# Kernel optimization log

Hardware: AMD Instinct MI355X
Metric: run time of the kernel (lower is better)

## Reference

```python
import jax, jax.numpy as jnp
import numpy as np

N = 20000      # total nodes
E = 160000     # total edges
G = 64         # graphs in batch
D_ESM = 1280
D = 512
OUT = 500
NUM_LAYERS = 3


def setup_inputs() -> dict:
    key = jax.random.key(0)
    ks = jax.random.split(key, 16)
    s = 0.02
    inp = {
        "native_x": jax.random.randint(ks[0], (N,), 0, 21),
        "x": jax.random.normal(ks[1], (N, D_ESM), dtype=jnp.float32),
        "edge_index": jax.random.randint(ks[2], (2, E), 0, N),
        "batch": jnp.sort(jax.random.randint(ks[3], (N,), 0, G)),
        # parameters
        "embed_table": jax.random.normal(ks[4], (21, 96), dtype=jnp.float32) * s,
        "proj_aa_w": jax.random.normal(ks[5], (96, D), dtype=jnp.float32) * s,
        "proj_aa_b": jnp.zeros((D,), jnp.float32),
        "proj_esm_w": jax.random.normal(ks[6], (D_ESM, D), dtype=jnp.float32) * s,
        "proj_esm_b": jnp.zeros((D,), jnp.float32),
        "gcn_w": jax.random.normal(ks[7], (NUM_LAYERS, D, D), dtype=jnp.float32) * s,
        "gcn_b": jnp.zeros((NUM_LAYERS, D), jnp.float32),
        "ro1_w": jax.random.normal(ks[8], (D, 1024), dtype=jnp.float32) * s,
        "ro1_b": jnp.zeros((1024,), jnp.float32),
        "ro2_w": jax.random.normal(ks[9], (1024, OUT), dtype=jnp.float32) * s,
        "ro2_b": jnp.zeros((OUT,), jnp.float32),
        "weight1": jnp.array([0.6, 0.4], jnp.float32),
    }
    return inp


def _gcn_stack(feat, src, dst, enorm, self_norm, gcn_w, gcn_b):
    # GraphCNN: 3 GCNConv layers (PyG: sym-normalized adj with self loops),
    # residual add after the first layer.
    for i in range(NUM_LAYERS):
        hW = feat @ gcn_w[i]                                   # [N, D]
        msg = hW[src] * enorm[:, None]                          # [E, D] gather
        agg = jax.ops.segment_sum(msg, dst, num_segments=N)     # scatter-add
        agg = agg + hW * self_norm[:, None] + gcn_b[i]
        out = jax.nn.relu(agg)
        feat = out if i == 0 else feat + out
    return feat


def reference(native_x, x, edge_index, batch, embed_table,
              proj_aa_w, proj_aa_b, proj_esm_w, proj_esm_b,
              gcn_w, gcn_b, ro1_w, ro1_b, ro2_w, ro2_b, weight1):
    # embedding + projections (dropout = identity, eval mode)
    x_aa = embed_table[native_x] @ proj_aa_w + proj_aa_b        # [N, 512]
    x_esm_lin = x @ proj_esm_w + proj_esm_b                     # [N, 512]
    h = jax.nn.relu(x_aa + x_esm_lin)
    x_esm = jax.nn.relu(x_esm_lin)

    src, dst = edge_index[0], edge_index[1]
    # GCN normalization with self loops: deg over targets + 1
    deg = jax.ops.segment_sum(jnp.ones((E,), x.dtype), dst, num_segments=N) + 1.0
    dis = deg ** -0.5
    enorm = dis[src] * dis[dst]     # per-edge norm
    self_norm = dis * dis           # self-loop norm

    n1 = _gcn_stack(h, src, dst, enorm, self_norm, gcn_w, gcn_b)
    n3 = _gcn_stack(x_esm, src, dst, enorm, self_norm, gcn_w, gcn_b)

    # global max pool per graph
    g1 = jax.ops.segment_max(n1, batch, num_segments=G)          # [G, 512]
    g3 = jax.ops.segment_max(n3, batch, num_segments=G)

    g = weight1[0] * g1 + weight1[1] * g3
    y = jax.nn.sigmoid(jax.nn.relu(g @ ro1_w + ro1_b) @ ro2_w + ro2_b)
    return y
```

## Files before the change

kernel.cpp:

```cpp
#include <hip/hip_runtime.h>
#include <float.h>

#define NN 20000
#define EE 160000
#define GG 64
#define DD 512
#define NL 3
#define M2 40000
#define M2P 40960
#define M1 20000
#define M1P 20480
#define BK 64

typedef __bf16 bf16x8 __attribute__((ext_vector_type(8)));
typedef float f32x4 __attribute__((ext_vector_type(4)));
typedef unsigned int u32;
typedef unsigned short u16;
typedef u32 u32x4 __attribute__((ext_vector_type(4)));
typedef u32 u32x2 __attribute__((ext_vector_type(2)));

union FragU { u32x4 u; bf16x8 b; };

__device__ inline float blo(u32 u){ union{u32 i;float f;}x; x.i=u<<16; return x.f; }
__device__ inline float bhi(u32 u){ union{u32 i;float f;}x; x.i=u&0xFFFF0000u; return x.f; }
__device__ inline u16 f2bf(float f){ union{float f;u32 i;}x; x.f=f; u32 r=x.i+0x7FFFu+((x.i>>16)&1u); return (u16)(r>>16); }
__device__ inline u32 pack2(float a,float b){ return (u32)f2bf(a) | ((u32)f2bf(b)<<16); }

__device__ __forceinline__ void gload16(const void* g, void* lds){
  __builtin_amdgcn_global_load_lds(
    (const __attribute__((address_space(1))) void*)g,
    (__attribute__((address_space(3))) void*)lds, 16, 0, 0);
}

__device__ __forceinline__ void acc8(float* a, uint4 q, float w){
  a[0]+=w*blo(q.x); a[1]+=w*bhi(q.x);
  a[2]+=w*blo(q.y); a[3]+=w*bhi(q.y);
  a[4]+=w*blo(q.z); a[5]+=w*bhi(q.z);
  a[6]+=w*blo(q.w); a[7]+=w*bhi(q.w);
}

__global__ void k_cvtdeg(const float* __restrict__ in, u16* __restrict__ outp,
                         const int* __restrict__ ei, int* __restrict__ deg){
  int b = blockIdx.x;
  if(b < 12800){
    int t = b*256+threadIdx.x;
    int row = t/160, gidx = t%160;
    u32x4 o;
    if(row < M1){
      const float* s = in + (size_t)row*1280 + gidx*8;
      float4 v0 = *(const float4*)s;
      float4 v1 = *(const float4*)(s+4);
      o.x=pack2(v0.x,v0.y); o.y=pack2(v0.z,v0.w);
      o.z=pack2(v1.x,v1.y); o.w=pack2(v1.z,v1.w);
    } else {
      o.x=o.y=o.z=o.w=0u;
    }
    *(u32x4*)(outp + (size_t)row*1280 + gidx*8) = o;
  } else {
    int e = (b-12800)*256+threadIdx.x;
    if(e<EE) atomicAdd(&deg[ei[EE+e]], 1);
  }
}

__device__ __forceinline__ void dev_tcvt(const float* __restrict__ in, u16* __restrict__ outp,
                                         int R, int C, int bx, int by, int tx, int ty, float* t){
  int c0 = bx*32, r0 = by*32;
  t[ty*33+tx] = in[(size_t)(r0+ty)*C + c0+tx];
  __syncthreads();
  outp[(size_t)(c0+ty)*R + r0+tx] = f2bf(t[tx*33+ty]);
}
__device__ __forceinline__ void dev_t32(const float* __restrict__ in, float* __restrict__ outp,
                                        int R, int C, int bx, int by, int tx, int ty, float* t){
  int c0 = bx*32, r0 = by*32;
  int r = r0+ty, c = c0+tx;
  if(r<R && c<C) t[ty*33+tx] = in[(size_t)r*C + c];
  __syncthreads();
  int oc = c0+ty, orr = r0+tx;
  if(oc<C && orr<R) outp[(size_t)oc*R + orr] = t[tx*33+ty];
}

__global__ __launch_bounds__(1024) void k_prep(const float* __restrict__ pesm_w, u16* __restrict__ WtE,
    const float* __restrict__ gcn_w, u16* __restrict__ WtG,
    const float* __restrict__ ro1_w, float* __restrict__ roT1,
    const float* __restrict__ ro2_w, float* __restrict__ roT2,
    const float* __restrict__ et, const float* __restrict__ paa_w,
    const float* __restrict__ paa_b, float* __restrict__ embp){
  __shared__ float t[32*33];
  int rb = blockIdx.x;
  int tid = threadIdx.x;
  int tx = tid&31, ty = tid>>5;
  if(rb < 640){ dev_tcvt(pesm_w, WtE, 1280, 512, rb%16, rb/16, tx, ty, t); return; }
  rb -= 640;
  if(rb < 768){
    int z = rb/256, r2 = rb%256;
    dev_tcvt(gcn_w + (size_t)z*262144, WtG + (size_t)z*262144, 512, 512, r2%16, r2/16, tx, ty, t);
    return;
  }
  rb -= 768;
  if(rb < 512){ dev_t32(ro1_w, roT1, 512, 1024, rb%32, rb/32, tx, ty, t); return; }
  rb -= 512;
  if(rb < 512){ dev_t32(ro2_w, roT2, 1024, 500, rb%16, rb/16, tx, ty, t); return; }
  rb -= 512;
  {
    int tt = rb*1024 + tid;
    if(tt < 21*512){
      int a = tt>>9, d = tt&511;
      float s = paa_b[d];
      for(int k=0;k<96;k++) s += et[a*96+k]*paa_w[k*512+d];
      embp[tt] = s;
    }
  }
}

__global__ __launch_bounds__(1024) void k_scanA(const int* __restrict__ deg, int* __restrict__ loff,
                        float* __restrict__ dis, const int* __restrict__ batch,
                        int* __restrict__ starts, int* __restrict__ bsum){
  __shared__ int ws[16];
  int b = blockIdx.x, tid = threadIdx.x;
  int n = b*1024 + tid;
  int lane = tid & 63, wv = tid >> 6;
  int dv = 0;
  if(n < NN){ dv = deg[n]; dis[n] = rsqrtf((float)dv + 1.0f); }
  int v = dv;
  #pragma unroll
  for(int off=1; off<64; off<<=1){
    int t = __shfl_up(v, off, 64);
    if(lane >= off) v += t;
  }
  if(lane==63) ws[wv] = v;
  __syncthreads();
  if(wv==0){
    int s = (lane<16)? ws[lane] : 0;
    #pragma unroll
    for(int off=1; off<16; off<<=1){
      int t = __shfl_up(s, off, 64);
      if(lane>=off) s += t;
    }
    if(lane<16) ws[lane] = s;
  }
  __syncthreads();
  int wbase = wv ? ws[wv-1] : 0;
  if(n < NN) loff[n] = wbase + v - dv;
  if(tid==1023) bsum[b] = ws[15];
  if(n < NN){
    int bb = batch[n];
    int pb = n ? batch[n-1] : -1;
    for(int g=pb+1; g<=bb; g++) starts[g]=n;
    if(n==NN-1){ for(int g=bb+1; g<=GG; g++) starts[g]=NN; }
  }
}
__global__ void k_scanB(const int* __restrict__ bsum, int* __restrict__ bbase){
  int lane = threadIdx.x;
  int x = (lane<20)? bsum[lane] : 0;
  int v = x;
  #pragma unroll
  for(int off=1; off<32; off<<=1){
    int t = __shfl_up(v, off, 64);
    if(lane>=off) v += t;
  }
  if(lane<20) bbase[lane] = v - x;
}
__global__ void k_scanC(const int* __restrict__ loff, const int* __restrict__ bbase,
                        int* __restrict__ offs){
  int n = blockIdx.x*1024 + threadIdx.x;
  if(n < NN) offs[n] = bbase[n>>10] + loff[n];
  if(n == 0) offs[NN] = EE;
}
__global__ void k_fill(const int* __restrict__ ei, const int* __restrict__ offs, int* __restrict__ curs,
                       const float* __restrict__ dis, int2* __restrict__ edat){
  int e = blockIdx.x*256+threadIdx.x; if(e>=EE) return;
  int s = ei[e], d = ei[EE+e];
  int pos = atomicAdd(&curs[d],1);
  edat[offs[d]+pos] = make_int2(s*2048, __float_as_int(dis[s]*dis[d]));
}

template<int EPI>
__global__ __launch_bounds__(256) void k_gemm(const u16* __restrict__ A, const u16* __restrict__ Bt,
                                              u16* __restrict__ C, int Mstore, int K, int lda,
                                              const int* __restrict__ nx, const float* __restrict__ embp,
                                              const float* __restrict__ esm_b){
  __shared__ u16 lsA[128*BK];
  __shared__ u16 lsB[128*BK];
  const int tid = threadIdx.x;
  const int lane = tid & 63;
  const int wid = tid >> 6;
  const int wr = wid >> 1, wc = wid & 1;
  const int la = lane & 15, lg = lane >> 4;
  const int w = blockIdx.x;
  const int xr = w & 7, kk2 = w >> 3;
  const int n0 = (kk2 & 3) * 128;
  const int rowB = (xr + 8*(kk2 >> 2)) * 128;

  f32x4 acc[4][4];
  #pragma unroll
  for(int m=0;m<4;m++)
    #pragma unroll
    for(int n=0;n<4;n++)
      #pragma unroll
      for(int r=0;r<4;r++) acc[m][n][r]=0.f;

  const u16* Arow = A + (size_t)rowB*lda;
  const u16* Brow = Bt + (size_t)n0*K;

  int srow[4], scol[4], ldsoff[4];
  #pragma unroll
  for(int i=0;i<4;i++){
    int li = i*256+tid;
    srow[i] = li>>3;
    scol[i] = ((li&7) ^ (srow[i]&7))*8;
    ldsoff[i] = (i*256 + wid*64)*8;
  }

  for(int k0=0;k0<K;k0+=BK){
    #pragma unroll
    for(int i=0;i<4;i++)
      gload16(Arow + (size_t)srow[i]*lda + k0 + scol[i], lsA + ldsoff[i]);
    #pragma unroll
    for(int i=0;i<4;i++)
      gload16(Brow + (size_t)srow[i]*K + k0 + scol[i], lsB + ldsoff[i]);
    __syncthreads();
    #pragma unroll
    for(int kk=0;kk<2;kk++){
      FragU aF[4], bF[4];
      #pragma unroll
      for(int m=0;m<4;m++){
        int row = wr*64+m*16+la;
        aF[m].u = *(const u32x4*)&lsA[row*BK + ((kk*4+lg)^(row&7))*8];
      }
      #pragma unroll
      for(int n=0;n<4;n++){
        int row = wc*64+n*16+la;
        bF[n].u = *(const u32x4*)&lsB[row*BK + ((kk*4+lg)^(row&7))*8];
      }
      #pragma unroll
      for(int m=0;m<4;m++)
        #pragma unroll
        for(int n=0;n<4;n++)
          acc[m][n] = __builtin_amdgcn_mfma_f32_16x16x32_bf16(aF[m].b, bF[n].b, acc[m][n], 0,0,0);
    }
    __syncthreads();
  }
  #pragma unroll
  for(int m=0;m<4;m++)
    #pragma unroll
    for(int r=0;r<4;r++){
      int rr = rowB + wr*64 + m*16 + lg*4 + r;
      if(rr < Mstore){
        int aidx = (EPI==1) ? nx[rr] : 0;
        #pragma unroll
        for(int n=0;n<4;n++){
          int col = n0 + wc*64 + n*16 + la;
          float v = acc[m][n][r];
          if(EPI==0){
            C[(size_t)rr*512 + col] = f2bf(v);
          } else {
            float t1 = v + esm_b[col];
            float hh = embp[aidx*512 + col] + t1;
            C[(size_t)(2*rr)*512 + col]   = f2bf(hh>0.f?hh:0.f);
            C[(size_t)(2*rr+1)*512 + col] = f2bf(t1>0.f?t1:0.f);
          }
        }
      }
    }
}

template<int MODE>
__global__ __launch_bounds__(256) void k_agg7(const u16* __restrict__ hW, u16* __restrict__ feat,
                 const int* __restrict__ offs, const int2* __restrict__ edat,
                 const float* __restrict__ dis, const float* __restrict__ bias){
  const int b = blockIdx.x;
  const int sl = b & 1;
  const int wv = threadIdx.x >> 6;
  const int lane = threadIdx.x & 63;
  const int nn = (b>>1)*4 + wv;
  const int co = sl*1024 + lane*16;
  const char* base = (const char*)hW;
  const int e0 = offs[nn], e1 = offs[nn+1];
  float a[8]={0,0,0,0,0,0,0,0};

  uint4 qs = *(const uint4*)(base + (size_t)nn*2048 + co);
  uint4 qf = make_uint4(0,0,0,0);
  if(MODE>0) qf = *(const uint4*)((const char*)feat + (size_t)nn*2048 + co);
  float dn = dis[nn], sn = dn*dn;

  int e = e0;
  for(; e+1 < e1; e += 2){
    int2 edA = edat[e], edB = edat[e+1];
    uint4 qA = *(const uint4*)(base + (u32)edA.x + co);
    uint4 qB = *(const uint4*)(base + (u32)edB.x + co);
    acc8(a, qA, __int_as_float(edA.y));
    acc8(a, qB, __int_as_float(edB.y));
  }
  if(e < e1){
    int2 edA = edat[e];
    uint4 qA = *(const uint4*)(base + (u32)edA.x + co);
    acc8(a, qA, __int_as_float(edA.y));
  }
  acc8(a, qs, sn);

  float4 b0 = *(const float4*)(bias + lane*8);
  float4 b1 = *(const float4*)(bias + lane*8 + 4);
  a[0]+=b0.x; a[1]+=b0.y; a[2]+=b0.z; a[3]+=b0.w;
  a[4]+=b1.x; a[5]+=b1.y; a[6]+=b1.z; a[7]+=b1.w;
  #pragma unroll
  for(int j=0;j<8;j++) a[j] = a[j]>0.f ? a[j] : 0.f;
  if(MODE>0) acc8(a, qf, 1.f);
  uint4 o;
  o.x=pack2(a[0],a[1]); o.y=pack2(a[2],a[3]);
  o.z=pack2(a[4],a[5]); o.w=pack2(a[6],a[7]);
  *(uint4*)((char*)feat + (size_t)nn*2048 + co) = o;
}

__global__ void k_pool(const u16* __restrict__ feat, const int* __restrict__ starts,
                       u32* __restrict__ m1, u32* __restrict__ m3){
  int g = blockIdx.x, c = blockIdx.y;
  int s = starts[g], e = starts[g+1];
  int len = e - s;
  int b0 = s + (len*c)/8, b1 = s + (len*(c+1))/8;
  int t = threadIdx.x;
  float a0=0.f, a1=0.f, c0=0.f, c1=0.f;
  for(int n=b0;n<b1;++n){
    const u16* pr = feat + (size_t)(2*n)*512 + t*2;
    u32 q1 = *(const u32*)pr;
    u32 q3 = *(const u32*)(pr + 512);
    a0 = fmaxf(a0, blo(q1)); a1 = fmaxf(a1, bhi(q1));
    c0 = fmaxf(c0, blo(q3)); c1 = fmaxf(c1, bhi(q3));
  }
  atomicMax(m1 + g*512 + t*2,     __float_as_uint(a0));
  atomicMax(m1 + g*512 + t*2 + 1, __float_as_uint(a1));
  atomicMax(m3 + g*512 + t*2,     __float_as_uint(c0));
  atomicMax(m3 + g*512 + t*2 + 1, __float_as_uint(c1));
}

__global__ __launch_bounds__(256) void k_ro1v(const u32* __restrict__ m1b, const u32* __restrict__ m3b,
                                              const float* __restrict__ w1, const float* __restrict__ wT,
                                              const float* __restrict__ b, float* __restrict__ r1){
  int gw = blockIdx.x*4 + (threadIdx.x>>6);
  int g = gw >> 10, o = gw & 1023;
  int lane = threadIdx.x & 63;
  float w10 = w1[0], w11 = w1[1];
  const uint4* g1 = (const uint4*)(m1b + (size_t)g*512);
  const uint4* g3 = (const uint4*)(m3b + (size_t)g*512);
  const float4* wr = (const float4*)(wT + (size_t)o*512);
  float s = 0.f;
  #pragma unroll
  for(int i=0;i<2;i++){
    uint4 q1 = g1[i*64+lane];
    uint4 q3 = g3[i*64+lane];
    float4 w = wr[i*64+lane];
    s += (w10*__uint_as_float(q1.x) + w11*__uint_as_float(q3.x))*w.x;
    s += (w10*__uint_as_float(q1.y) + w11*__uint_as_float(q3.y))*w.y;
    s += (w10*__uint_as_float(q1.z) + w11*__uint_as_float(q3.z))*w.z;
    s += (w10*__uint_as_float(q1.w) + w11*__uint_as_float(q3.w))*w.w;
  }
  #pragma unroll
  for(int m=32;m>=1;m>>=1) s += __shfl_xor(s, m, 64);
  if(lane==0){ s += b[o]; r1[gw] = s>0.f ? s : 0.f; }
}
__global__ __launch_bounds__(256) void k_ro2v(const float* __restrict__ r1, const float* __restrict__ wT,
                                              const float* __restrict__ b, float* __restrict__ y){
  int gw = blockIdx.x*4 + (threadIdx.x>>6);
  int g = gw/500, o = gw - g*500;
  int lane = threadIdx.x & 63;
  const float4* gr = (const float4*)(r1 + (size_t)g*1024);
  const float4* wr = (const float4*)(wT + (size_t)o*1024);
  float s = 0.f;
  #pragma unroll
  for(int i=0;i<4;i++){
    float4 a = gr[i*64+lane];
    float4 w = wr[i*64+lane];
    s += a.x*w.x + a.y*w.y + a.z*w.z + a.w*w.w;
  }
  #pragma unroll
  for(int m=32;m>=1;m>>=1) s += __shfl_xor(s, m, 64);
  if(lane==0) y[gw] = 1.0f/(1.0f+__expf(-(s + b[o])));
}

extern "C" void kernel_launch(void* const* d_in, const int* in_sizes, int n_in,
                              void* d_out, int out_size, void* d_ws, size_t ws_size,
                              hipStream_t stream){
  const int*   native_x = (const int*)d_in[0];
  const float* x        = (const float*)d_in[1];
  const int*   ei       = (const int*)d_in[2];
  const int*   batch    = (const int*)d_in[3];
  const float* embed_t  = (const float*)d_in[4];
  const float* paa_w    = (const float*)d_in[5];
  const float* paa_b    = (const float*)d_in[6];
  const float* pesm_w   = (const float*)d_in[7];
  const float* pesm_b   = (const float*)d_in[8];
  const float* gcn_w    = (const float*)d_in[9];
  const float* gcn_b    = (const float*)d_in[10];
  const float* ro1_w    = (const float*)d_in[11];
  const float* ro1_b    = (const float*)d_in[12];
  const float* ro2_w    = (const float*)d_in[13];
  const float* ro2_b    = (const float*)d_in[14];
  const float* w1       = (const float*)d_in[15];
  float* out = (float*)d_out;

  char* p = (char*)d_ws;
  auto alloc = [&](size_t n){ void* r = (void*)p; p += (n + 255) & ~(size_t)255; return r; };
  u16* feat   = (u16*)alloc((size_t)M2P*512*2);
  u16* hW     = (u16*)alloc((size_t)M2P*512*2);
  u16* xbf    = (u16*)alloc((size_t)M1P*1280*2);
  u16* WtE    = (u16*)alloc((size_t)512*1280*2);
  u16* WtG    = (u16*)alloc((size_t)3*512*512*2);
  float* roT1 = (float*)alloc((size_t)1024*512*4);
  float* roT2 = (float*)alloc((size_t)500*1024*4);
  float* embp = (float*)alloc(21*512*4);
  int* deg    = (int*)alloc(NN*4);
  int* curs   = (int*)alloc(NN*4);
  float* dis  = (float*)alloc(NN*4);
  int* loff   = (int*)alloc(NN*4);
  int* offs   = (int*)alloc((NN+1)*4);
  int* bsum   = (int*)alloc(32*4);
  int* bbase  = (int*)alloc(32*4);
  int2* edat  = (int2*)alloc((size_t)EE*8);
  int* starts = (int*)alloc((GG+1)*4);
  u32* m1b    = (u32*)alloc(GG*512*4);
  u32* m3b    = (u32*)alloc(GG*512*4);
  float* r1   = (float*)alloc(GG*1024*4);
  (void)ws_size; (void)in_sizes; (void)n_in; (void)out_size;

  hipMemsetAsync(deg, 0, ((NN*4+255)&~(size_t)255) + NN*4, stream);
  hipMemsetAsync(m1b, 0, 2*GG*512*4, stream);

  k_cvtdeg<<<12800+625,256,0,stream>>>(x, xbf, ei, deg);
  k_prep<<<640+768+512+512+11,1024,0,stream>>>(pesm_w, WtE, gcn_w, WtG, ro1_w, roT1, ro2_w, roT2,
                                               embed_t, paa_w, paa_b, embp);
  k_scanA<<<20,1024,0,stream>>>(deg, loff, dis, batch, starts, bsum);
  k_scanB<<<1,64,0,stream>>>(bsum, bbase);
  k_scanC<<<20,1024,0,stream>>>(loff, bbase, offs);
  k_fill<<<(EE+255)/256,256,0,stream>>>(ei, offs, curs, dis, edat);

  k_gemm<1><<<4*(M1P/128),256,0,stream>>>(xbf, WtE, feat, M1, 1280, 1280, native_x, embp, pesm_b);

  k_gemm<0><<<4*(M2P/128),256,0,stream>>>(feat, WtG,            hW, M2, 512, 512, nullptr, nullptr, nullptr);
  k_agg7<0><<<NN/2,256,0,stream>>>(hW, feat, offs, edat, dis, gcn_b);
  k_gemm<0><<<4*(M2P/128),256,0,stream>>>(feat, WtG+262144,     hW, M2, 512, 512, nullptr, nullptr, nullptr);
  k_agg7<1><<<NN/2,256,0,stream>>>(hW, feat, offs, edat, dis, gcn_b+512);
  k_gemm<0><<<4*(M2P/128),256,0,stream>>>(feat, WtG+2*262144,   hW, M2, 512, 512, nullptr, nullptr, nullptr);
  k_agg7<1><<<NN/2,256,0,stream>>>(hW, feat, offs, edat, dis, gcn_b+1024);

  k_pool<<<dim3(GG,8),256,0,stream>>>(feat, starts, m1b, m3b);
  k_ro1v<<<16384,256,0,stream>>>(m1b, m3b, w1, roT1, ro1_b, r1);
  k_ro2v<<<8000,256,0,stream>>>(r1, roT2, ro2_b, out);
}
```

Baseline: 398.2 us.

## Rewrite GEMM as 256x256-tile, 8-wave kernel with double-buffered LDS pipeline

Result: slower. 437.4 us (+9.8%).

```diff
diff --git a/kernel.cpp b/kernel.cpp
--- a/kernel.cpp
+++ b/kernel.cpp
@@ -174,77 +174,127 @@
   edat[offs[d]+pos] = make_int2(s*2048, __float_as_int(dis[s]*dis[d]));
 }
 
+#define ASM_VMCNT4 asm volatile("s_waitcnt vmcnt(4)" ::: "memory")
+#define ASM_VMCNT0 asm volatile("s_waitcnt vmcnt(0)" ::: "memory")
+#define ASM_LGKM0  asm volatile("s_waitcnt lgkmcnt(0)" ::: "memory")
+
 template<int EPI>
-__global__ __launch_bounds__(256) void k_gemm(const u16* __restrict__ A, const u16* __restrict__ Bt,
+__global__ __launch_bounds__(512,2) void k_gemm8(const u16* __restrict__ A, const u16* __restrict__ Bt,
                                               u16* __restrict__ C, int Mstore, int K, int lda,
                                               const int* __restrict__ nx, const float* __restrict__ embp,
                                               const float* __restrict__ esm_b){
-  __shared__ u16 lsA[128*BK];
-  __shared__ u16 lsB[128*BK];
+  __shared__ u16 ls[8*8192];
   const int tid = threadIdx.x;
   const int lane = tid & 63;
   const int wid = tid >> 6;
-  const int wr = wid >> 1, wc = wid & 1;
+  const int wr = wid >> 2;
+  const int wc = wid & 3;
   const int la = lane & 15, lg = lane >> 4;
   const int w = blockIdx.x;
   const int xr = w & 7, kk2 = w >> 3;
-  const int n0 = (kk2 & 3) * 128;
-  const int rowB = (xr + 8*(kk2 >> 2)) * 128;
-
-  f32x4 acc[4][4];
-  #pragma unroll
-  for(int m=0;m<4;m++)
+  const int n0 = (kk2 & 1) * 256;
+  const int rowB = (xr + 8*(kk2 >> 1)) * 256;
+  const int nt = K >> 6;
+
+  const u16* Arow = A + (size_t)rowB*lda;
+  const u16* Brow = Bt + (size_t)n0*K;
+
+  f32x4 acc[8][4];
+  #pragma unroll
+  for(int m=0;m<8;m++)
     #pragma unroll
     for(int n=0;n<4;n++)
       #pragma unroll
       for(int r=0;r<4;r++) acc[m][n][r]=0.f;
 
-  const u16* Arow = A + (size_t)rowB*lda;
-  const u16* Brow = Bt + (size_t)n0*K;
-
-  int srow[4], scol[4], ldsoff[4];
-  #pragma unroll
-  for(int i=0;i<4;i++){
-    int li = i*256+tid;
-    srow[i] = li>>3;
-    scol[i] = ((li&7) ^ (srow[i]&7))*8;
-    ldsoff[i] = (i*256 + wid*64)*8;
-  }
-
-  for(int k0=0;k0<K;k0+=BK){
-    #pragma unroll
-    for(int i=0;i<4;i++)
-      gload16(Arow + (size_t)srow[i]*lda + k0 + scol[i], lsA + ldsoff[i]);
-    #pragma unroll
-    for(int i=0;i<4;i++)
-      gload16(Brow + (size_t)srow[i]*K + k0 + scol[i], lsB + ldsoff[i]);
-    __syncthreads();
-    #pragma unroll
-    for(int kk=0;kk<2;kk++){
-      FragU aF[4], bF[4];
-      #pragma unroll
-      for(int m=0;m<4;m++){
-        int row = wr*64+m*16+la;
-        aF[m].u = *(const u32x4*)&lsA[row*BK + ((kk*4+lg)^(row&7))*8];
-      }
-      #pragma unroll
-      for(int n=0;n<4;n++){
-        int row = wc*64+n*16+la;
-        bF[n].u = *(const u32x4*)&lsB[row*BK + ((kk*4+lg)^(row&7))*8];
-      }
-      #pragma unroll
-      for(int m=0;m<4;m++)
-        #pragma unroll
-        for(int n=0;n<4;n++)
-          acc[m][n] = __builtin_amdgcn_mfma_f32_16x16x32_bf16(aF[m].b, bF[n].b, acc[m][n], 0,0,0);
-    }
-    __syncthreads();
-  }
-  #pragma unroll
-  for(int m=0;m<4;m++)
+  int srow[2], sgc[2];
+  #pragma unroll
+  for(int j=0;j<2;j++){
+    int s = j*512+tid;
+    srow[j] = s>>2;
+    sgc[j]  = ((s&3) ^ ((srow[j]>>1)&3))*8;
+  }
+
+#define PANEL(buf,mat,kh) (ls + (((buf)*2+(mat))*2+(kh))*8192)
+#define STAGE(buf,mat,kh,kt) { \
+    const u16* _src = (mat)? Brow : Arow; \
+    int _ld = (mat)? K : lda; \
+    int _k0 = (kt)*64 + (kh)*32; \
+    u16* _dst = PANEL(buf,mat,kh); \
+    _Pragma("unroll") \
+    for(int _j=0;_j<2;_j++) \
+      gload16(_src + (size_t)srow[_j]*_ld + _k0 + sgc[_j], _dst + (_j*512+tid)*8); \
+  }
+#define LDA4(f,buf,kh,qm) { \
+    const u16* _pa = PANEL(buf,0,kh); \
+    _Pragma("unroll") \
+    for(int _m=0;_m<4;_m++){ \
+      int _row = wr*128 + (qm)*64 + _m*16 + la; \
+      f[_m].u = *(const u32x4*)(_pa + _row*32 + ((lg ^ ((_row>>1)&3))*8)); \
+    } \
+  }
+#define LDB4(f,buf,kh) { \
+    const u16* _pb = PANEL(buf,1,kh); \
+    _Pragma("unroll") \
+    for(int _n=0;_n<4;_n++){ \
+      int _row = wc*64 + _n*16 + la; \
+      f[_n].u = *(const u32x4*)(_pb + _row*32 + ((lg ^ ((_row>>1)&3))*8)); \
+    } \
+  }
+#define MM16(af,bf,qm) { \
+    _Pragma("unroll") \
+    for(int _m=0;_m<4;_m++) \
+      _Pragma("unroll") \
+      for(int _n=0;_n<4;_n++) \
+        acc[(qm)*4+_m][_n] = __builtin_amdgcn_mfma_f32_16x16x32_bf16(af[_m].b, bf[_n].b, acc[(qm)*4+_m][_n], 0,0,0); \
+  }
+
+  STAGE(0,0,0,0); STAGE(0,1,0,0); STAGE(0,0,1,0); STAGE(0,1,1,0);
+  ASM_VMCNT4;
+  __builtin_amdgcn_s_barrier();
+
+  for(int t=0;t<nt;t++){
+    const int c = t&1;
+    const bool st = (t+1 < nt);
+    const bool lastt = (t == nt-1);
+    FragU aF[4], b0F[4], b1F[4];
+
+    LDA4(aF, c, 0, 0); LDB4(b0F, c, 0);
+    if(st) STAGE(c^1, 0, 0, t+1);
+    __builtin_amdgcn_s_barrier();
+    ASM_LGKM0; __builtin_amdgcn_sched_barrier(0);
+    __builtin_amdgcn_s_setprio(1); MM16(aF, b0F, 0); __builtin_amdgcn_s_setprio(0);
+    __builtin_amdgcn_s_barrier();
+
+    LDA4(aF, c, 0, 1);
+    if(st) STAGE(c^1, 1, 0, t+1);
+    if(lastt){ ASM_VMCNT0; } else { ASM_VMCNT4; }
+    __builtin_amdgcn_s_barrier();
+    ASM_LGKM0; __builtin_amdgcn_sched_barrier(0);
+    __builtin_amdgcn_s_setprio(1); MM16(aF, b0F, 1); __builtin_amdgcn_s_setprio(0);
+    __builtin_amdgcn_s_barrier();
+
+    LDA4(aF, c, 1, 0); LDB4(b1F, c, 1);
+    if(st) STAGE(c^1, 0, 1, t+1);
+    __builtin_amdgcn_s_barrier();
+    ASM_LGKM0; __builtin_amdgcn_sched_barrier(0);
+    __builtin_amdgcn_s_setprio(1); MM16(aF, b1F, 0); __builtin_amdgcn_s_setprio(0);
+    __builtin_amdgcn_s_barrier();
+
+    LDA4(aF, c, 1, 1);
+    if(st) STAGE(c^1, 1, 1, t+1);
+    if(!lastt){ ASM_VMCNT4; }
+    __builtin_amdgcn_s_barrier();
+    ASM_LGKM0; __builtin_amdgcn_sched_barrier(0);
+    __builtin_amdgcn_s_setprio(1); MM16(aF, b1F, 1); __builtin_amdgcn_s_setprio(0);
+    __builtin_amdgcn_s_barrier();
+  }
+
+  #pragma unroll
+  for(int m=0;m<8;m++)
     #pragma unroll
     for(int r=0;r<4;r++){
-      int rr = rowB + wr*64 + m*16 + lg*4 + r;
+      int rr = rowB + wr*128 + m*16 + lg*4 + r;
       if(rr < Mstore){
         int aidx = (EPI==1) ? nx[rr] : 0;
         #pragma unroll
@@ -262,6 +312,11 @@
         }
       }
     }
+#undef PANEL
+#undef STAGE
+#undef LDA4
+#undef LDB4
+#undef MM16
 }
 
 template<int MODE>
@@ -432,13 +487,13 @@
   k_scanC<<<20,1024,0,stream>>>(loff, bbase, offs);
   k_fill<<<(EE+255)/256,256,0,stream>>>(ei, offs, curs, dis, edat);
 
-  k_gemm<1><<<4*(M1P/128),256,0,stream>>>(xbf, WtE, feat, M1, 1280, 1280, native_x, embp, pesm_b);
-
-  k_gemm<0><<<4*(M2P/128),256,0,stream>>>(feat, WtG,            hW, M2, 512, 512, nullptr, nullptr, nullptr);
+  k_gemm8<1><<<2*(M1P/256),512,0,stream>>>(xbf, WtE, feat, M1, 1280, 1280, native_x, embp, pesm_b);
+
+  k_gemm8<0><<<2*(M2P/256),512,0,stream>>>(feat, WtG,            hW, M2, 512, 512, nullptr, nullptr, nullptr);
   k_agg7<0><<<NN/2,256,0,stream>>>(hW, feat, offs, edat, dis, gcn_b);
-  k_gemm<0><<<4*(M2P/128),256,0,stream>>>(feat, WtG+262144,     hW, M2, 512, 512, nullptr, nullptr, nullptr);
+  k_gemm8<0><<<2*(M2P/256),512,0,stream>>>(feat, WtG+262144,     hW, M2, 512, 512, nullptr, nullptr, nullptr);
   k_agg7<1><<<NN/2,256,0,stream>>>(hW, feat, offs, edat, dis, gcn_b+512);
-  k_gemm<0><<<4*(M2P/128),256,0,stream>>>(feat, WtG+2*262144,   hW, M2, 512, 512, nullptr, nullptr, nullptr);
+  k_gemm8<0><<<2*(M2P/256),512,0,stream>>>(feat, WtG+2*262144,   hW, M2, 512, 512, nullptr, nullptr, nullptr);
   k_agg7<1><<<NN/2,256,0,stream>>>(hW, feat, offs, edat, dis, gcn_b+1024);
 
   k_pool<<<dim3(GG,8),256,0,stream>>>(feat, starts, m1b, m3b);
```
